# Performance work log

Measured on AMD Instinct MI355X. Metric: run time of the kernel, lower is better.

The kernel has to match this reference:

```python
import jax, jax.numpy as jnp
import numpy as np

D_MODEL = 1024
N_HEADS = 16
HEAD_DIM = D_MODEL // N_HEADS
EPS = 1e-6


def setup_inputs() -> dict:
    key = jax.random.key(0)
    ks = jax.random.split(key, 10)
    s = 0.02
    return {
        "sequence": jax.random.normal(ks[0], (4, 2048, D_MODEL), dtype=jnp.float32),
        "ln_gamma": jnp.ones((D_MODEL,), jnp.float32),
        "ln_beta": jnp.zeros((D_MODEL,), jnp.float32),
        "Wq": jax.random.normal(ks[1], (D_MODEL, D_MODEL), jnp.float32) * s,
        "bq": jnp.zeros((D_MODEL,), jnp.float32),
        "Wk": jax.random.normal(ks[2], (D_MODEL, D_MODEL), jnp.float32) * s,
        "bk": jnp.zeros((D_MODEL,), jnp.float32),
        "Wv": jax.random.normal(ks[3], (D_MODEL, D_MODEL), jnp.float32) * s,
        "bv": jnp.zeros((D_MODEL,), jnp.float32),
        "Wo": jax.random.normal(ks[4], (D_MODEL, D_MODEL), jnp.float32) * s,
        "bo": jnp.zeros((D_MODEL,), jnp.float32),
        "mu": jnp.zeros((1, 1, 1, 1), jnp.float32),
    }


def _split_heads(x):
    b, s, d = x.shape
    return x.reshape(b, s, N_HEADS, HEAD_DIM).transpose(0, 2, 1, 3)  # [B,H,S,hd]


def reference(sequence, ln_gamma, ln_beta, Wq, bq, Wk, bk, Wv, bv, Wo, bo, mu):
    # LayerNorm (eps=1e-6)
    mean = jnp.mean(sequence, axis=-1, keepdims=True)
    var = jnp.mean(jnp.square(sequence - mean), axis=-1, keepdims=True)
    x = (sequence - mean) / jnp.sqrt(var + EPS) * ln_gamma + ln_beta

    # QKV projections (torch Linear: x @ W.T + b)
    q = _split_heads(x @ Wq.T + bq)
    k = _split_heads(x @ Wk.T + bk)
    v = _split_heads(x @ Wv.T + bv)

    scale = HEAD_DIM ** 0.5
    scores = jnp.einsum("bhqd,bhkd->bhqk", q, k) / scale  # [B,H,S,S]
    scores = jax.nn.sigmoid(scores - mu) * jnp.exp(scores)
    scores = scores / jnp.sum(scores, axis=-1, keepdims=True)

    out = jnp.einsum("bhqk,bhkd->bhqd", scores, v)  # [B,H,S,hd]
    b, h, s, hd = out.shape
    out = out.transpose(0, 2, 1, 3).reshape(b, s, h * hd)
    return out @ Wo.T + bo  # dropout is identity at inference
```

## Files before the change

kernel.cpp:

```cpp
#include <hip/hip_runtime.h>
#include <hip/hip_bf16.h>
#include <cstdint>
#include <cstddef>


typedef __bf16 bf16_t;
typedef __bf16 bf16x4 __attribute__((ext_vector_type(4)));
typedef __bf16 bf16x8 __attribute__((ext_vector_type(8)));
typedef float  f32x4  __attribute__((ext_vector_type(4)));
typedef float  f32x16 __attribute__((ext_vector_type(16)));
typedef unsigned u32x4 __attribute__((ext_vector_type(4)));

#define MFMA16(a, b, c) __builtin_amdgcn_mfma_f32_16x16x32_bf16((a), (b), (c), 0, 0, 0)
#define MFMA32(a, b, c) __builtin_amdgcn_mfma_f32_32x32x16_bf16((a), (b), (c), 0, 0, 0)

#if __has_builtin(__builtin_amdgcn_exp2f)
#define VEXP2(x) __builtin_amdgcn_exp2f(x)
#else
#define VEXP2(x) __expf((x) * 0.6931471805599453f)
#endif

__device__ __forceinline__ unsigned cvtpk_bf16(float a, float b) {
  unsigned r;
  asm("v_cvt_pk_bf16_f32 %0, %1, %2" : "=v"(r) : "v"(a), "v"(b));
  return r;
}

__device__ __forceinline__ void plane32_swap(unsigned& a, unsigned& b) {
  asm volatile("v_permlane32_swap_b32 %0, %1" : "+v"(a), "+v"(b));
}

__device__ __forceinline__ void gload16(void* lds, const void* g) {
  __builtin_amdgcn_global_load_lds(
      (__attribute__((address_space(1))) void*)(uintptr_t)g,
      (__attribute__((address_space(3))) void*)(uint32_t)(uintptr_t)lds,
      16, 0, 0);
}

__global__ __launch_bounds__(256) void prep_k(
    const float* __restrict__ s0, const float* __restrict__ s1,
    const float* __restrict__ s2, const float* __restrict__ s3,
    bf16_t* __restrict__ wdst,
    const float* __restrict__ x, const float* __restrict__ gamma,
    const float* __restrict__ beta, bf16_t* __restrict__ xout)
{
  int bid = blockIdx.x;
  int tid = threadIdx.x;
  if (bid < 4096) {
    int part = bid >> 10;
    const float* src = part == 0 ? s0 : part == 1 ? s1 : part == 2 ? s2 : s3;
    int i = (bid & 1023) * 256 + tid;
    float4 v = ((const float4*)src)[i];
    bf16x4 o = { (bf16_t)v.x, (bf16_t)v.y, (bf16_t)v.z, (bf16_t)v.w };
    *(bf16x4*)(wdst + (((size_t)part) << 20) + (size_t)i * 4) = o;
  } else {
    int row = bid - 4096;
    float4 v = ((const float4*)(x + (size_t)row * 1024))[tid];
    float s  = v.x + v.y + v.z + v.w;
    float ss = v.x * v.x + v.y * v.y + v.z * v.z + v.w * v.w;
#pragma unroll
    for (int m = 1; m < 64; m <<= 1) { s += __shfl_xor(s, m); ss += __shfl_xor(ss, m); }
    __shared__ float sh_s[4], sh_q[4];
    int w = tid >> 6;
    if ((tid & 63) == 0) { sh_s[w] = s; sh_q[w] = ss; }
    __syncthreads();
    s  = sh_s[0] + sh_s[1] + sh_s[2] + sh_s[3];
    ss = sh_q[0] + sh_q[1] + sh_q[2] + sh_q[3];
    float mean = s * (1.0f / 1024.0f);
    float var  = ss * (1.0f / 1024.0f) - mean * mean;
    float rstd = rsqrtf(var + 1e-6f);
    float4 gv = ((const float4*)gamma)[tid];
    float4 bv = ((const float4*)beta)[tid];
    bf16x4 o = { (bf16_t)((v.x - mean) * rstd * gv.x + bv.x),
                 (bf16_t)((v.y - mean) * rstd * gv.y + bv.y),
                 (bf16_t)((v.z - mean) * rstd * gv.z + bv.z),
                 (bf16_t)((v.w - mean) * rstd * gv.w + bv.w) };
    *(bf16x4*)(xout + (size_t)row * 1024 + tid * 4) = o;
  }
}

__global__ __launch_bounds__(256) void gemm_bt(
    const bf16_t* __restrict__ A, const bf16_t* __restrict__ Bw,
    const float* __restrict__ b0, const float* __restrict__ b1,
    const float* __restrict__ b2,
    void* __restrict__ o0, void* __restrict__ o1, void* __restrict__ o2,
    int M, int N, int K, int fused)
{
  __shared__ __align__(16) bf16_t a_lds[2][128][32];
  __shared__ __align__(16) bf16_t b_lds[2][128][32];
  const int tid = threadIdx.x;
  const int l = tid & 63, w = tid >> 6;
  const int wr = w >> 1, wc = w & 1;
  const int m0 = blockIdx.y * 128, n0 = blockIdx.x * 128;
  const int lr = l & 15, lg = l >> 4;

  f32x4 acc[4][4] = {};

  const int srow = tid >> 2;
  const int scol = (tid & 3) * 8;
  const bf16_t* ag = A  + (size_t)(m0 + srow) * K + scol;
  const bf16_t* bg = Bw + (size_t)(n0 + srow) * K + scol;

  gload16((char*)a_lds[0] + tid * 16,        ag);
  gload16((char*)a_lds[0] + 4096 + tid * 16, ag + (size_t)64 * K);
  gload16((char*)b_lds[0] + tid * 16,        bg);
  gload16((char*)b_lds[0] + 4096 + tid * 16, bg + (size_t)64 * K);
  __syncthreads();

  int cur = 0;
  for (int k0 = 0; k0 < K; k0 += 32) {
    if (k0 + 32 < K) {
      gload16((char*)a_lds[cur ^ 1] + tid * 16,        ag + k0 + 32);
      gload16((char*)a_lds[cur ^ 1] + 4096 + tid * 16, ag + (size_t)64 * K + k0 + 32);
      gload16((char*)b_lds[cur ^ 1] + tid * 16,        bg + k0 + 32);
      gload16((char*)b_lds[cur ^ 1] + 4096 + tid * 16, bg + (size_t)64 * K + k0 + 32);
    }
    bf16x8 af[4], bf[4];
#pragma unroll
    for (int i = 0; i < 4; ++i) {
      af[i] = *(const bf16x8*)&a_lds[cur][wr * 64 + i * 16 + lr][lg * 8];
      bf[i] = *(const bf16x8*)&b_lds[cur][wc * 64 + i * 16 + lr][lg * 8];
    }
#pragma unroll
    for (int i = 0; i < 4; ++i)
#pragma unroll
      for (int j = 0; j < 4; ++j)
        acc[i][j] = MFMA16(af[i], bf[j], acc[i][j]);
    __syncthreads();
    cur ^= 1;
  }

  int matsel = fused ? (n0 >> 10) : 0;
  const float* bias = matsel == 0 ? b0 : matsel == 1 ? b1 : b2;
  float bs[4];
#pragma unroll
  for (int j = 0; j < 4; ++j) bs[j] = bias[(n0 + wc * 64 + j * 16 + lr) & 1023];

#pragma unroll
  for (int i = 0; i < 4; ++i) {
#pragma unroll
    for (int j = 0; j < 4; ++j) {
      if (fused && matsel == 2) {
        int row0 = m0 + wr * 64 + i * 16 + lg * 4;
        int col  = n0 + wc * 64 + j * 16 + lr;
        int nn = col & 1023;
        int bb = row0 >> 11, s0 = row0 & 2047, hh = nn >> 6, d = nn & 63;
        bf16x4 pv;
#pragma unroll
        for (int r = 0; r < 4; ++r) pv[r] = (bf16_t)(acc[i][j][r] + bs[j]);
        *(bf16x4*)((bf16_t*)o2 + ((((size_t)bb * 16 + hh) * 64) + d) * 2048 + s0) = pv;
      } else {
#pragma unroll
        for (int r = 0; r < 4; ++r) {
          int row = m0 + wr * 64 + i * 16 + lg * 4 + r;
          int col = n0 + wc * 64 + j * 16 + lr;
          float v = acc[i][j][r] + bs[j];
          if (!fused) {
            ((float*)o0)[(size_t)row * N + col] = v;
          } else {
            int nn = col & 1023;
            int bb = row >> 11, s = row & 2047, hh = nn >> 6, d = nn & 63;
            bf16_t* o = matsel ? (bf16_t*)o1 : (bf16_t*)o0;
            if (matsel == 0) v *= 0.18033688011112042f;
            o[((((size_t)bb * 16 + hh) * 2048 + s) << 6) + d] = (bf16_t)v;
          }
        }
      }
    }
  }
}

#define ATTN_TILE(T_, ISSUE_, VM_)                                            \
  {                                                                           \
    if (ISSUE_) {                                                             \
      gload16((char*)k_lds[((T_) + 2) & 3] + tid * 16,                        \
              kbase + koff + ((T_) + 2) * 8192);                              \
      gload16((char*)v_lds[((T_) + 2) & 3] + tid * 16,                        \
              vbase + voff + ((T_) + 2) * 128);                               \
    }                                                                         \
    asm volatile("s_waitcnt vmcnt(" #VM_ ")" ::: "memory");                   \
    __builtin_amdgcn_s_barrier();                                             \
    __builtin_amdgcn_sched_barrier(0);                                        \
    const char* kldsb_ = (const char*)k_lds[(T_) & 3];                        \
    const char* vldsb_ = (const char*)v_lds[(T_) & 3];                        \
    _Pragma("unroll")                                                         \
    for (int kh = 0; kh < 2; ++kh) {                                          \
      f32x16 sc = {};                                                         \
      __builtin_amdgcn_s_setprio(1);                                          \
      _Pragma("unroll")                                                       \
      for (int ch = 0; ch < 4; ++ch) {                                        \
        bf16x8 kf = *(const bf16x8*)(kldsb_ + (kh * 32 + l31) * 128           \
                                     + ((ch * 32 + hi * 16) ^ swzr));         \
        sc = MFMA32(kf, qf[ch], sc);                                          \
      }                                                                       \
      __builtin_amdgcn_s_setprio(0);                                          \
      unsigned U[8];                                                          \
      _Pragma("unroll")                                                       \
      for (int m = 0; m < 8; ++m) {                                           \
        float t0 = VEXP2(-sc[2 * m]);                                         \
        float t1 = VEXP2(-sc[2 * m + 1]);                                     \
        float d0 = fmaf(emu * t0, t0, t0);                                    \
        float d1 = fmaf(emu * t1, t1, t1);                                    \
        float inv = __builtin_amdgcn_rcpf(d0 * d1);                           \
        float w0 = inv * d1;                                                  \
        float w1 = inv * d0;                                                  \
        rs0 += w0; rs1 += w1;                                                 \
        U[m] = cvtpk_bf16(w0, w1);                                            \
      }                                                                       \
      plane32_swap(U[0], U[2]);                                               \
      plane32_swap(U[1], U[3]);                                               \
      plane32_swap(U[4], U[6]);                                               \
      plane32_swap(U[5], U[7]);                                               \
      __builtin_amdgcn_s_setprio(1);                                          \
      _Pragma("unroll")                                                       \
      for (int cc = 0; cc < 2; ++cc) {                                        \
        u32x4 uu = { U[cc * 4 + 0], U[cc * 4 + 1], U[cc * 4 + 2],             \
                     U[cc * 4 + 3] };                                         \
        bf16x8 pa = __builtin_bit_cast(bf16x8, uu);                           \
        int kcol = (kh * 2 + cc) * 32 + hi * 16;                              \
        _Pragma("unroll")                                                     \
        for (int df = 0; df < 2; ++df) {                                      \
          bf16x8 vf = *(const bf16x8*)(vldsb_ + (df * 32 + l31) * 128         \
                                       + (kcol ^ swzr));                      \
          oAcc[df] = MFMA32(pa, vf, oAcc[df]);                                \
        }                                                                     \
      }                                                                       \
      __builtin_amdgcn_s_setprio(0);                                          \
    }                                                                         \
  }

__global__ __launch_bounds__(512) void attn_k(
    const bf16_t* __restrict__ q, const bf16_t* __restrict__ k,
    const bf16_t* __restrict__ vT, const float* __restrict__ mu_p,
    bf16_t* __restrict__ out)
{
  const int S = 2048;
  int hw = blockIdx.x;
  int vid = (hw & 7) * 64 + (hw >> 3);
  int qt = vid & 7;
  int bh = vid >> 3;
  int h = bh & 15, b = bh >> 4;

  const bf16_t* qb = q  + ((size_t)bh * S + qt * 256) * 64;
  const char* kbase = (const char*)(k  + (size_t)bh * S * 64);
  const char* vbase = (const char*)(vT + (size_t)bh * 64 * S);
  const float emu = __expf(mu_p[0]);

  __shared__ __align__(16) bf16_t k_lds[4][64][64];
  __shared__ __align__(16) bf16_t v_lds[4][64][64];

  const int tid = threadIdx.x, l = tid & 63, w = tid >> 6;
  const int l31 = l & 31, hi = l >> 5;
  const int swzr = (l31 & 7) << 4;

  bf16x8 qf[4];
#pragma unroll
  for (int ch = 0; ch < 4; ++ch)
    qf[ch] = *(const bf16x8*)(qb + (size_t)(w * 32 + l31) * 64 + ch * 16 + hi * 8);

  const int srow = tid >> 3;
  const int ssw  = ((tid & 7) * 16) ^ ((srow & 7) << 4);
  const int koff = srow * 128 + ssw;
  const int voff = srow * 4096 + ssw;

  f32x16 oAcc[2] = {};
  float rs0 = 0.f, rs1 = 0.f;

  gload16((char*)k_lds[0] + tid * 16, kbase + koff);
  gload16((char*)v_lds[0] + tid * 16, vbase + voff);
  gload16((char*)k_lds[1] + tid * 16, kbase + koff + 8192);
  gload16((char*)v_lds[1] + tid * 16, vbase + voff + 128);

#pragma unroll 4
  for (int t = 0; t < 28; ++t) ATTN_TILE(t, true, 4);
  ATTN_TILE(28, true, 4);
  ATTN_TILE(29, true, 4);
  ATTN_TILE(30, false, 2);
  ATTN_TILE(31, false, 0);

  float rs = rs0 + rs1;
  rs += __shfl_xor(rs, 32);
  float rinv = __builtin_amdgcn_rcpf(rs);

#pragma unroll
  for (int r = 0; r < 16; ++r) {
    int q_loc = (r & 3) + 8 * (r >> 2) + 4 * hi;
    float ro = __shfl(rinv, q_loc);
    size_t row = (size_t)b * 2048 + qt * 256 + w * 32 + q_loc;
#pragma unroll
    for (int df = 0; df < 2; ++df) {
      out[row * 1024 + h * 64 + df * 32 + l31] = (bf16_t)(oAcc[df][r] * ro);
    }
  }
}

extern "C" void kernel_launch(void* const* d_in, const int* in_sizes, int n_in,
                              void* d_out, int out_size, void* d_ws, size_t ws_size,
                              hipStream_t stream) {
  const float* seq = (const float*)d_in[0];
  const float* g   = (const float*)d_in[1];
  const float* be  = (const float*)d_in[2];
  const float* Wq  = (const float*)d_in[3];
  const float* bq  = (const float*)d_in[4];
  const float* Wk  = (const float*)d_in[5];
  const float* bk  = (const float*)d_in[6];
  const float* Wv  = (const float*)d_in[7];
  const float* bv  = (const float*)d_in[8];
  const float* Wo  = (const float*)d_in[9];
  const float* bo  = (const float*)d_in[10];
  const float* mu  = (const float*)d_in[11];

  char* ws = (char*)d_ws;
  bf16_t* xb   = (bf16_t*)ws;  ws += (size_t)8192 * 1024 * 2;
  bf16_t* wAll = (bf16_t*)ws;  ws += (size_t)4 * 1024 * 1024 * 2;
  bf16_t* qb   = (bf16_t*)ws;  ws += (size_t)8192 * 1024 * 2;
  bf16_t* kbuf = (bf16_t*)ws;  ws += (size_t)8192 * 1024 * 2;
  bf16_t* vtb  = (bf16_t*)ws;  ws += (size_t)8192 * 1024 * 2;
  bf16_t* ab   = (bf16_t*)ws;  ws += (size_t)8192 * 1024 * 2;
  bf16_t* wqkv = wAll;
  bf16_t* wob  = wAll + (size_t)3 * 1024 * 1024;

  dim3 blk(256);
  prep_k<<<dim3(12288), blk, 0, stream>>>(Wq, Wk, Wv, Wo, wAll, seq, g, be, xb);
  gemm_bt<<<dim3(24, 64), blk, 0, stream>>>(xb, wqkv, bq, bk, bv,
                                            qb, kbuf, vtb, 8192, 3072, 1024, 1);
  attn_k<<<dim3(512), dim3(512), 0, stream>>>(qb, kbuf, vtb, mu, ab);
  gemm_bt<<<dim3(8, 64), blk, 0, stream>>>(ab, wob, bo, nullptr, nullptr,
                                           d_out, nullptr, nullptr, 8192, 1024, 1024, 0);
}
```

Before: 207.3 us.

## Rewrite projection GEMM with 256x128 tiles, swizzled LDS, phased pipelining and XCD remap

Replaces the 128x128, K=32 GEMM with a 512-thread kernel that uses 256x128 output tiles and a K step of 64. LDS rows are XOR-swizzled to avoid bank conflicts, and each K tile is split into two phases that interleave the async global loads with the MFMAs, using explicit vmcnt waits, barriers and setprio. Block IDs are remapped so that neighbouring tiles land on the same XCD, which should improve L2 reuse. The kernel hardcodes K=1024 and M=8192 strides, which makes it less general, and it uses more LDS per block.

```diff
diff --git a/kernel.cpp b/kernel.cpp
--- a/kernel.cpp
+++ b/kernel.cpp
@@ -79,70 +79,115 @@
   }
 }
 
-__global__ __launch_bounds__(256) void gemm_bt(
+#define G_PHASE(T_, P_, ISSUE_, VM_, DOVM_)                                   \
+  {                                                                           \
+    if (ISSUE_) {                                                             \
+      const char* asrc_ = ag + ((T_) + 1) * 128;                              \
+      const char* bsrc_ = bg + ((T_) + 1) * 128;                              \
+      char* adst_ = (char*)a_lds[((T_) + 1) & 1] + tid * 16;                  \
+      char* bdst_ = (char*)b_lds[((T_) + 1) & 1] + tid * 16;                  \
+      if ((P_) == 0) {                                                        \
+        gload16(adst_,         asrc_);                                        \
+        gload16(adst_ + 8192,  asrc_ + 131072);                               \
+        gload16(bdst_,         bsrc_);                                        \
+      } else {                                                                \
+        gload16(adst_ + 16384, asrc_ + 262144);                               \
+        gload16(adst_ + 24576, asrc_ + 393216);                               \
+        gload16(bdst_ + 8192,  bsrc_ + 131072);                               \
+      }                                                                       \
+    }                                                                         \
+    if (DOVM_) { asm volatile("s_waitcnt vmcnt(" VM_ ")" ::: "memory"); }     \
+    __builtin_amdgcn_s_barrier();                                             \
+    __builtin_amdgcn_sched_barrier(0);                                        \
+    const char* al_ = (const char*)a_lds[(T_) & 1];                           \
+    const char* bl_ = (const char*)b_lds[(T_) & 1];                           \
+    if ((P_) == 0) {                                                          \
+      _Pragma("unroll")                                                       \
+      for (int j = 0; j < 4; ++j)                                             \
+        _Pragma("unroll")                                                     \
+        for (int ks = 0; ks < 2; ++ks)                                        \
+          bf[j][ks] = *(const bf16x8*)(bl_ + (wn * 64 + j * 16 + lr) * 128    \
+                          + ((ks * 64 + lg * 16) ^ swzr));                    \
+    }                                                                         \
+    _Pragma("unroll")                                                         \
+    for (int ri = 0; ri < 2; ++ri) {                                          \
+      const int i_ = (P_) * 2 + ri;                                           \
+      bf16x8 af0 = *(const bf16x8*)(al_ + (wm * 64 + i_ * 16 + lr) * 128      \
+                        + ((lg * 16) ^ swzr));                                \
+      bf16x8 af1 = *(const bf16x8*)(al_ + (wm * 64 + i_ * 16 + lr) * 128      \
+                        + ((64 + lg * 16) ^ swzr));                           \
+      __builtin_amdgcn_s_setprio(1);                                          \
+      _Pragma("unroll")                                                       \
+      for (int j = 0; j < 4; ++j) {                                           \
+        acc[i_][j] = MFMA16(af0, bf[j][0], acc[i_][j]);                       \
+        acc[i_][j] = MFMA16(af1, bf[j][1], acc[i_][j]);                       \
+      }                                                                       \
+      __builtin_amdgcn_s_setprio(0);                                          \
+    }                                                                         \
+    __builtin_amdgcn_s_barrier();                                             \
+  }
+
+#define G_TILE(T_, ISSUE_, VM0_)     \
+  G_PHASE(T_, 0, ISSUE_, VM0_, true) \
+  G_PHASE(T_, 1, ISSUE_, "0", false)
+
+__global__ __launch_bounds__(512) void gemm256(
     const bf16_t* __restrict__ A, const bf16_t* __restrict__ Bw,
     const float* __restrict__ b0, const float* __restrict__ b1,
     const float* __restrict__ b2,
     void* __restrict__ o0, void* __restrict__ o1, void* __restrict__ o2,
-    int M, int N, int K, int fused)
+    int nbx, int N, int fused)
 {
-  __shared__ __align__(16) bf16_t a_lds[2][128][32];
-  __shared__ __align__(16) bf16_t b_lds[2][128][32];
-  const int tid = threadIdx.x;
-  const int l = tid & 63, w = tid >> 6;
-  const int wr = w >> 1, wc = w & 1;
-  const int m0 = blockIdx.y * 128, n0 = blockIdx.x * 128;
+  __shared__ __align__(16) bf16_t a_lds[2][256][64];
+  __shared__ __align__(16) bf16_t b_lds[2][128][64];
+  const int tid = threadIdx.x, l = tid & 63, wid = tid >> 6;
+  const int wm = wid >> 1, wn = wid & 1;
   const int lr = l & 15, lg = l >> 4;
+  const int swzr = (lr & 7) << 4;
+
+  int hw = blockIdx.x;
+  int cpx = (nbx * 32) >> 3;
+  int vid = (hw & 7) * cpx + (hw >> 3);
+  int by = vid / nbx, bx = vid % nbx;
+  const int m0 = by * 256, n0 = bx * 128;
 
   f32x4 acc[4][4] = {};
 
-  const int srow = tid >> 2;
-  const int scol = (tid & 3) * 8;
-  const bf16_t* ag = A  + (size_t)(m0 + srow) * K + scol;
-  const bf16_t* bg = Bw + (size_t)(n0 + srow) * K + scol;
-
-  gload16((char*)a_lds[0] + tid * 16,        ag);
-  gload16((char*)a_lds[0] + 4096 + tid * 16, ag + (size_t)64 * K);
-  gload16((char*)b_lds[0] + tid * 16,        bg);
-  gload16((char*)b_lds[0] + 4096 + tid * 16, bg + (size_t)64 * K);
-  __syncthreads();
-
-  int cur = 0;
-  for (int k0 = 0; k0 < K; k0 += 32) {
-    if (k0 + 32 < K) {
-      gload16((char*)a_lds[cur ^ 1] + tid * 16,        ag + k0 + 32);
-      gload16((char*)a_lds[cur ^ 1] + 4096 + tid * 16, ag + (size_t)64 * K + k0 + 32);
-      gload16((char*)b_lds[cur ^ 1] + tid * 16,        bg + k0 + 32);
-      gload16((char*)b_lds[cur ^ 1] + 4096 + tid * 16, bg + (size_t)64 * K + k0 + 32);
-    }
-    bf16x8 af[4], bf[4];
-#pragma unroll
-    for (int i = 0; i < 4; ++i) {
-      af[i] = *(const bf16x8*)&a_lds[cur][wr * 64 + i * 16 + lr][lg * 8];
-      bf[i] = *(const bf16x8*)&b_lds[cur][wc * 64 + i * 16 + lr][lg * 8];
-    }
-#pragma unroll
-    for (int i = 0; i < 4; ++i)
-#pragma unroll
-      for (int j = 0; j < 4; ++j)
-        acc[i][j] = MFMA16(af[i], bf[j], acc[i][j]);
-    __syncthreads();
-    cur ^= 1;
+  const int srow = tid >> 3;
+  const int ssw  = ((tid & 7) * 16) ^ ((srow & 7) << 4);
+  const char* ag = (const char*)A  + (size_t)(m0 + srow) * 2048 + ssw;
+  const char* bg = (const char*)Bw + (size_t)(n0 + srow) * 2048 + ssw;
+
+  gload16((char*)a_lds[0] + tid * 16,         ag);
+  gload16((char*)a_lds[0] + 8192 + tid * 16,  ag + 131072);
+  gload16((char*)a_lds[0] + 16384 + tid * 16, ag + 262144);
+  gload16((char*)a_lds[0] + 24576 + tid * 16, ag + 393216);
+  gload16((char*)b_lds[0] + tid * 16,         bg);
+  gload16((char*)b_lds[0] + 8192 + tid * 16,  bg + 131072);
+
+#pragma unroll 2
+  for (int t = 0; t < 15; ++t) {
+    bf16x8 bf[4][2];
+    G_TILE(t, true, "3");
+  }
+  {
+    bf16x8 bf[4][2];
+    G_TILE(15, false, "0");
   }
 
   int matsel = fused ? (n0 >> 10) : 0;
   const float* bias = matsel == 0 ? b0 : matsel == 1 ? b1 : b2;
   float bs[4];
 #pragma unroll
-  for (int j = 0; j < 4; ++j) bs[j] = bias[(n0 + wc * 64 + j * 16 + lr) & 1023];
+  for (int j = 0; j < 4; ++j) bs[j] = bias[(n0 + wn * 64 + j * 16 + lr) & 1023];
 
 #pragma unroll
   for (int i = 0; i < 4; ++i) {
 #pragma unroll
     for (int j = 0; j < 4; ++j) {
       if (fused && matsel == 2) {
-        int row0 = m0 + wr * 64 + i * 16 + lg * 4;
-        int col  = n0 + wc * 64 + j * 16 + lr;
+        int row0 = m0 + wm * 64 + i * 16 + lg * 4;
+        int col  = n0 + wn * 64 + j * 16 + lr;
         int nn = col & 1023;
         int bb = row0 >> 11, s0 = row0 & 2047, hh = nn >> 6, d = nn & 63;
         bf16x4 pv;
@@ -152,8 +197,8 @@
       } else {
 #pragma unroll
         for (int r = 0; r < 4; ++r) {
-          int row = m0 + wr * 64 + i * 16 + lg * 4 + r;
-          int col = n0 + wc * 64 + j * 16 + lr;
+          int row = m0 + wm * 64 + i * 16 + lg * 4 + r;
+          int col = n0 + wn * 64 + j * 16 + lr;
           float v = acc[i][j][r] + bs[j];
           if (!fused) {
             ((float*)o0)[(size_t)row * N + col] = v;
@@ -320,11 +365,10 @@
   bf16_t* wqkv = wAll;
   bf16_t* wob  = wAll + (size_t)3 * 1024 * 1024;
 
-  dim3 blk(256);
-  prep_k<<<dim3(12288), blk, 0, stream>>>(Wq, Wk, Wv, Wo, wAll, seq, g, be, xb);
-  gemm_bt<<<dim3(24, 64), blk, 0, stream>>>(xb, wqkv, bq, bk, bv,
-                                            qb, kbuf, vtb, 8192, 3072, 1024, 1);
+  prep_k<<<dim3(12288), dim3(256), 0, stream>>>(Wq, Wk, Wv, Wo, wAll, seq, g, be, xb);
+  gemm256<<<dim3(768), dim3(512), 0, stream>>>(xb, wqkv, bq, bk, bv,
+                                               qb, kbuf, vtb, 24, 3072, 1);
   attn_k<<<dim3(512), dim3(512), 0, stream>>>(qb, kbuf, vtb, mu, ab);
-  gemm_bt<<<dim3(8, 64), blk, 0, stream>>>(ab, wob, bo, nullptr, nullptr,
-                                           d_out, nullptr, nullptr, 8192, 1024, 1024, 0);
-}
+  gemm256<<<dim3(256), dim3(512), 0, stream>>>(ab, wob, bo, nullptr, nullptr,
+                                               d_out, nullptr, nullptr, 8, 1024, 0);
+}
```

Result: faster. 196.0 us, median of 3 (-5.4%).
